# Optimization experiments

Hardware: AMD Instinct MI355X
Metric: run time of the kernel (lower is better)

Reference implementation:

```python
import jax, jax.numpy as jnp
import numpy as np

WIN = 9
EPS = 1e-05


def _box3d(x, win=WIN):
    """Sum over a win^3 box (zero-padded), equivalent to conv3d with a ones kernel.
    Implemented as three separable 1D convolutions (exact same math, O(win)/voxel)."""
    pad = win // 2
    for axis in range(3):  # spatial axes D, H, W
        kshape = [1, 1, 1, 1, 1]
        kshape[2 + axis] = win
        kern = jnp.ones(kshape, x.dtype)
        pads = [(0, 0)] * 3
        pads[axis] = (pad, pad)
        dn = jax.lax.conv_dimension_numbers(x.shape, kern.shape, ('NCDHW', 'OIDHW', 'NCDHW'))
        x = jax.lax.conv_general_dilated(x, kern, window_strides=(1, 1, 1),
                                         padding=pads, dimension_numbers=dn)
    return x


def setup_inputs() -> dict:
    key = jax.random.key(0)
    k1, k2 = jax.random.split(key)
    shape = (1, 1, 160, 192, 224)  # [N, C, D, H, W] brain-MRI-scale volume
    I = jax.random.normal(k1, shape, dtype=jnp.float32)
    J = jax.random.normal(k2, shape, dtype=jnp.float32)
    return {"I": I, "J": J}


def reference(I, J):
    win_size = WIN ** 3
    I2 = I * I
    J2 = J * J
    IJ = I * J
    I_sum = _box3d(I)
    J_sum = _box3d(J)
    I2_sum = _box3d(I2)
    J2_sum = _box3d(J2)
    IJ_sum = _box3d(IJ)
    u_I = I_sum / win_size
    u_J = J_sum / win_size
    cross = IJ_sum - u_J * I_sum - u_I * J_sum + u_I * u_J * win_size
    I_var = I2_sum - 2 * u_I * I_sum + u_I * u_I * win_size
    J_var = J2_sum - 2 * u_J * J_sum + u_J * u_J * win_size
    cc = cross * cross / (I_var * J_var + EPS)
    return -1.0 * jnp.mean(cc)
```

## Files before the change

kernel.cpp:

```cpp
#include <hip/hip_runtime.h>


#define DD 160
#define HH 192
#define WW 224
#define W4 56
#define SLICE (HH * WW)
#define S4 (SLICE / 4)
#define NVOX (DD * SLICE)
#define TW 32
#define TH 16
#define DCH 19
#define ITERS (DCH + 8)
#define NTHR 512
#define SW_RS 36
#define SW_CS (24 * SW_RS)
#define EPS 1e-5f
#define INV_WSUM (1.0f / 729.0f)

__device__ __forceinline__ void bar_lds_only() {
    __asm__ volatile("" ::: "memory");
    __builtin_amdgcn_s_waitcnt(0xC07F);
    __builtin_amdgcn_s_barrier();
    __asm__ volatile("" ::: "memory");
}

__global__ __launch_bounds__(NTHR, 4) void ncc_fused(const float* __restrict__ I,
                                                     const float* __restrict__ J,
                                                     float* __restrict__ out) {
    __shared__ float SW0[5 * SW_CS], SW1[5 * SW_CS];
    __shared__ float SH[TH * TW * 5];
    __shared__ float wred[NTHR / 64];

    const int tid = threadIdx.x;
    const int tx = tid & 31, ty = tid >> 5;
    const int wlo = blockIdx.x * TW;
    const int hlo = blockIdx.y * TH;
    const int dlo = blockIdx.z * DCH;

    const int wr = tid >> 3, wc = tid & 7;
    const int gh = hlo - 4 + wr;
    const bool hok = (gh >= 0) && (gh < HH);
    const int gf0 = (wlo >> 2) - 1 + wc;

    const int ht = tid - 192;
    const int hcol = ht & 31, hch = ht >> 5;

    const float4* Iv = (const float4*)I;
    const float4* Jv = (const float4*)J;

    float pfa[12], pfb[12];

    auto w_load = [&](int z) {
        const bool zok = (z >= 0) && (z < DD) && hok;
        const int rowb = z * S4 + gh * W4;
        #pragma unroll
        for (int k = 0; k < 3; ++k) {
            const int f = gf0 + k;
            float4 a = make_float4(0.f, 0.f, 0.f, 0.f);
            float4 b = make_float4(0.f, 0.f, 0.f, 0.f);
            if (zok && f >= 0 && f < W4) { a = Iv[rowb + f]; b = Jv[rowb + f]; }
            pfa[4*k] = a.x; pfa[4*k+1] = a.y; pfa[4*k+2] = a.z; pfa[4*k+3] = a.w;
            pfb[4*k] = b.x; pfb[4*k+1] = b.y; pfb[4*k+2] = b.z; pfb[4*k+3] = b.w;
        }
    };

    auto w_compute = [&](float* dst) {
        float* wp = dst + wr * SW_RS + 4 * wc;
        #pragma unroll
        for (int ch = 0; ch < 5; ++ch) {
            float v[12];
            #pragma unroll
            for (int k = 0; k < 12; ++k)
                v[k] = (ch == 0) ? pfa[k]
                     : (ch == 1) ? pfb[k]
                     : (ch == 2) ? pfa[k] * pfa[k]
                     : (ch == 3) ? pfb[k] * pfb[k]
                     :             pfa[k] * pfb[k];
            float s = v[0];
            #pragma unroll
            for (int k = 1; k < 9; ++k) s += v[k];
            float4 o;
            o.x = s;
            s += v[9]  - v[0]; o.y = s;
            s += v[10] - v[1]; o.z = s;
            s += v[11] - v[2]; o.w = s;
            *(float4*)(wp + ch * SW_CS) = o;
        }
    };

    float q0[9], q1[9], q2[9], q3[9], q4[9];
    #pragma unroll
    for (int k = 0; k < 9; ++k) { q0[k]=0.f; q1[k]=0.f; q2[k]=0.f; q3[k]=0.f; q4[k]=0.f; }
    float r0=0.f, r1=0.f, r2=0.f, r3=0.f, r4=0.f;
    float acc = 0.f;

    if (tid < 192) {
        w_load(dlo - 4);
        if (dlo >= 4) w_compute(SW0);
        w_load(dlo - 3);
    }
    bar_lds_only();

    #pragma unroll 1
    for (int g = 0; g < 3; ++g) {
        #pragma unroll
        for (int ph = 0; ph < 9; ++ph) {
            const int i = 9 * g + ph;
            const int z = dlo - 4 + i;
            const bool val = (z >= 0) && (z < DD);
            const int par = i & 1;
            float* swR = par ? SW1 : SW0;
            float* swW = par ? SW0 : SW1;

            if (tid < 192) {
                if (i < ITERS - 1) {
                    const int zn = z + 1;
                    if (zn >= 0 && zn < DD) w_compute(swW);
                    w_load(z + 2);
                }
            } else if (ht < 160 && val) {
                const float* p = swR + hch * SW_CS + hcol;
                float v[24];
                #pragma unroll
                for (int r = 0; r < 24; r += 2) {
                    const float* pr = p + r * SW_RS;
                    v[r]     = pr[0];
                    v[r + 1] = pr[SW_RS];
                }
                float s = v[0];
                #pragma unroll
                for (int r = 1; r < 9; ++r) s += v[r];
                float* o = SH + hcol * 5 + hch;
                float prev = s;
                o[0] = s;
                #pragma unroll
                for (int r = 1; r < 16; ++r) {
                    prev += v[r + 8] - v[r - 1];
                    o[r * (TW * 5)] = prev;
                }
            }
            bar_lds_only();

            float w0=0.f, w1=0.f, w2=0.f, w3=0.f, w4=0.f;
            if (val) {
                const float* p = SH + (ty * TW + tx) * 5;
                w0 = p[0]; w1 = p[1]; w2 = p[2]; w3 = p[3]; w4 = p[4];
            }
            r0 += w0 - q0[ph]; q0[ph] = w0;
            r1 += w1 - q1[ph]; q1[ph] = w1;
            r2 += w2 - q2[ph]; q2[ph] = w2;
            r3 += w3 - q3[ph]; q3[ph] = w3;
            r4 += w4 - q4[ph]; q4[ph] = w4;

            if (i >= 8 && (dlo + i - 8) < DD) {
                float cross = r4 - r0 * r1 * INV_WSUM;
                float iv    = r2 - r0 * r0 * INV_WSUM;
                float jv    = r3 - r1 * r1 * INV_WSUM;
                acc += cross * cross * __builtin_amdgcn_rcpf(iv * jv + EPS);
            }
            bar_lds_only();
        }
    }

    #pragma unroll
    for (int off = 32; off > 0; off >>= 1) acc += __shfl_down(acc, off, 64);
    if ((tid & 63) == 0) wred[tid >> 6] = acc;
    __syncthreads();
    if (tid == 0) {
        float t = 0.f;
        #pragma unroll
        for (int k = 0; k < NTHR / 64; ++k) t += wred[k];
        atomicAdd(out, t * (-1.0f / (float)NVOX));
    }
}

extern "C" void kernel_launch(void* const* d_in, const int* in_sizes, int n_in,
                              void* d_out, int out_size, void* d_ws, size_t ws_size,
                              hipStream_t stream) {
    const float* I = (const float*)d_in[0];
    const float* J = (const float*)d_in[1];
    float* out = (float*)d_out;

    hipMemsetAsync(d_out, 0, sizeof(float), stream);

    dim3 blk(NTHR, 1, 1);
    dim3 grd(WW / TW, HH / TH, (DD + DCH - 1) / DCH);
    ncc_fused<<<grd, blk, 0, stream>>>(I, J, out);
}
```

Baseline: 136.8 us.

## Single-buffer W-pass LDS staging to cut shared memory per block

Replaces the double-buffered W-sum LDS arrays with a single buffer. W-sums are computed into registers while the H-pass reads the buffer, then stored after the barrier, and the next global load is moved after that store. This roughly halves LDS use per block so more blocks can be resident per CU. In exchange it adds register pressure and shortens the distance between issuing a global load and using it.

Measured after the change: 184.2 us. +34.7%, slower.

```diff
diff --git a/kernel.cpp b/kernel.cpp
--- a/kernel.cpp
+++ b/kernel.cpp
@@ -28,7 +28,7 @@
 __global__ __launch_bounds__(NTHR, 4) void ncc_fused(const float* __restrict__ I,
                                                      const float* __restrict__ J,
                                                      float* __restrict__ out) {
-    __shared__ float SW0[5 * SW_CS], SW1[5 * SW_CS];
+    __shared__ float SW[5 * SW_CS];
     __shared__ float SH[TH * TW * 5];
     __shared__ float wred[NTHR / 64];
 
@@ -50,6 +50,7 @@
     const float4* Jv = (const float4*)J;
 
     float pfa[12], pfb[12];
+    float ws[20];
 
     auto w_load = [&](int z) {
         const bool zok = (z >= 0) && (z < DD) && hok;
@@ -65,8 +66,7 @@
         }
     };
 
-    auto w_compute = [&](float* dst) {
-        float* wp = dst + wr * SW_RS + 4 * wc;
+    auto w_comp = [&]() {
         #pragma unroll
         for (int ch = 0; ch < 5; ++ch) {
             float v[12];
@@ -80,13 +80,19 @@
             float s = v[0];
             #pragma unroll
             for (int k = 1; k < 9; ++k) s += v[k];
-            float4 o;
-            o.x = s;
-            s += v[9]  - v[0]; o.y = s;
-            s += v[10] - v[1]; o.z = s;
-            s += v[11] - v[2]; o.w = s;
-            *(float4*)(wp + ch * SW_CS) = o;
+            ws[4*ch] = s;
+            s += v[9]  - v[0]; ws[4*ch+1] = s;
+            s += v[10] - v[1]; ws[4*ch+2] = s;
+            s += v[11] - v[2]; ws[4*ch+3] = s;
         }
+    };
+
+    auto w_store = [&]() {
+        float* wp = SW + wr * SW_RS + 4 * wc;
+        #pragma unroll
+        for (int ch = 0; ch < 5; ++ch)
+            *(float4*)(wp + ch * SW_CS) =
+                make_float4(ws[4*ch], ws[4*ch+1], ws[4*ch+2], ws[4*ch+3]);
     };
 
     float q0[9], q1[9], q2[9], q3[9], q4[9];
@@ -97,7 +103,7 @@
 
     if (tid < 192) {
         w_load(dlo - 4);
-        if (dlo >= 4) w_compute(SW0);
+        if (dlo >= 4) { w_comp(); w_store(); }
         w_load(dlo - 3);
     }
     bar_lds_only();
@@ -109,18 +115,12 @@
             const int i = 9 * g + ph;
             const int z = dlo - 4 + i;
             const bool val = (z >= 0) && (z < DD);
-            const int par = i & 1;
-            float* swR = par ? SW1 : SW0;
-            float* swW = par ? SW0 : SW1;
+            const bool nxt = (i < ITERS - 1) && (z + 1 >= 0) && (z + 1 < DD);
 
             if (tid < 192) {
-                if (i < ITERS - 1) {
-                    const int zn = z + 1;
-                    if (zn >= 0 && zn < DD) w_compute(swW);
-                    w_load(z + 2);
-                }
+                if (nxt) w_comp();
             } else if (ht < 160 && val) {
-                const float* p = swR + hch * SW_CS + hcol;
+                const float* p = SW + hch * SW_CS + hcol;
                 float v[24];
                 #pragma unroll
                 for (int r = 0; r < 24; r += 2) {
@@ -142,6 +142,10 @@
             }
             bar_lds_only();
 
+            if (tid < 192) {
+                if (nxt) w_store();
+                if (i < ITERS - 2) w_load(z + 2);
+            }
             float w0=0.f, w1=0.f, w2=0.f, w3=0.f, w4=0.f;
             if (val) {
                 const float* p = SH + (ty * TW + tx) * 5;
```
